# Kernel optimization log

Hardware: AMD Instinct MI355X
Metric: run time of the kernel (lower is better)

The kernel has to match this reference:

```python
import jax, jax.numpy as jnp
import numpy as np

N = 50000   # nodes
E = 800000  # edges
H = 128     # hidden_dim
H2 = H // 2


def setup_inputs() -> dict:
    key = jax.random.key(0)
    ks = jax.random.split(key, 12)
    s = 0.05  # weight scale for numerical sanity
    d = {}
    d['coord_x'] = jax.random.normal(ks[0], (N,), jnp.float32)
    d['coord_y'] = jax.random.normal(ks[1], (N,), jnp.float32)
    d['W1'] = jax.random.normal(ks[2], (3, H), jnp.float32) * s
    d['b1'] = jnp.zeros((H,), jnp.float32)
    d['W2'] = jax.random.normal(ks[3], (H, H), jnp.float32) * s
    d['b2'] = jnp.zeros((H,), jnp.float32)
    d['W3'] = jax.random.normal(ks[4], (H, H), jnp.float32) * s
    d['b3'] = jnp.zeros((H,), jnp.float32)
    d['W4'] = jax.random.normal(ks[5], (H, H), jnp.float32) * s
    d['b4'] = jnp.zeros((H,), jnp.float32)
    d['W5'] = jax.random.normal(ks[6], (H, H), jnp.float32) * s
    d['b5'] = jnp.zeros((H,), jnp.float32)
    d['Wl1'] = jax.random.normal(ks[7], (H, H2), jnp.float32) * s
    d['bl1'] = jnp.zeros((H2,), jnp.float32)
    d['Wl2'] = jax.random.normal(ks[8], (H2, 1), jnp.float32) * s
    d['bl2'] = jnp.zeros((1,), jnp.float32)
    d['src'] = jax.random.randint(ks[9], (E,), 0, N, dtype=jnp.int32)
    d['dst'] = jax.random.randint(ks[10], (E,), 0, N, dtype=jnp.int32)
    return d


def reference(coord_x, coord_y, W1, b1, W2, b2, W3, b3, W4, b4, W5, b5,
              Wl1, bl1, Wl2, bl2, src, dst):
    ones_e = jnp.ones((E,), jnp.float32)
    in_deg = jax.ops.segment_sum(ones_e, dst, num_segments=N)   # [N]
    out_deg = jax.ops.segment_sum(ones_e, src, num_segments=N)  # [N]
    # DGL GraphConv norm='both': D_out^{-1/2} on src side, D_in^{-1/2} on dst side,
    # degrees clamped to min 1.
    norm_s = (jnp.maximum(out_deg, 1.0) ** -0.5)[:, None]  # [N,1]
    norm_d = (jnp.maximum(in_deg, 1.0) ** -0.5)[:, None]   # [N,1]

    def gconv(h, W, b):
        msg = (h * norm_s)[src]                                   # [E,F] gather
        agg = jax.ops.segment_sum(msg, dst, num_segments=N)       # [N,F] scatter-add
        return (agg * norm_d) @ W + b

    # node features: [in_degree, x, y]
    h = jnp.stack([in_deg, coord_x, coord_y], axis=1)  # [N,3]
    for W, b in ((W1, b1), (W2, b2), (W3, b3), (W4, b4), (W5, b5)):
        h = jax.nn.relu(gconv(h, W, b))

    graph_emb = jnp.mean(h, axis=0, keepdims=True)          # [1,H] mean_nodes
    h_emb = jax.nn.relu(graph_emb @ Wl1 + bl1)              # dropout p=0 -> identity
    pred = jax.nn.sigmoid(h_emb @ Wl2 + bl2)                # [1,1]
    return pred, graph_emb, h
```

## Files before the change

kernel.cpp:

```cpp
#include <hip/hip_runtime.h>
#include <hip/hip_bf16.h>
#include <math.h>

#define NN 50000
#define NE 800000
#define HD 128
#define NB 196
#define CAP 5120
#define B1_EPB 1024

typedef __attribute__((ext_vector_type(8))) short bf16x8v;
typedef __attribute__((ext_vector_type(4))) float f32x4v;

static __device__ __forceinline__ unsigned short f2bf(float x) {
    union { float f; unsigned u; } v; v.f = x;
    unsigned r = v.u + 0x7fff + ((v.u >> 16) & 1);
    return (unsigned short)(r >> 16);
}

__global__ __launch_bounds__(256) void bucket_kernel(const int* __restrict__ src,
                                                     const int* __restrict__ dst,
                                                     int* __restrict__ dcur,
                                                     int* __restrict__ scur,
                                                     ushort2* __restrict__ dbucket,
                                                     unsigned short* __restrict__ sbucket) {
    __shared__ int hd[NB], hsb[NB], cd[NB], cs[NB];
    int t = threadIdx.x;
    if (t < NB) { hd[t] = 0; hsb[t] = 0; }
    __syncthreads();
    int d[4], s[4];
    int e0 = blockIdx.x * B1_EPB + t;
    #pragma unroll
    for (int j = 0; j < 4; ++j) {
        int e = e0 + j * 256;
        if (e < NE) {
            d[j] = dst[e]; s[j] = src[e];
            atomicAdd(&hd[d[j] >> 8], 1);
            atomicAdd(&hsb[s[j] >> 8], 1);
        } else d[j] = -1;
    }
    __syncthreads();
    if (t < NB) {
        cd[t] = atomicAdd(&dcur[t], hd[t]);
        cs[t] = atomicAdd(&scur[t], hsb[t]);
    }
    __syncthreads();
    #pragma unroll
    for (int j = 0; j < 4; ++j) {
        if (d[j] >= 0) {
            int b = d[j] >> 8;
            int p = atomicAdd(&cd[b], 1);
            if (p < CAP) dbucket[(long)b * CAP + p] = make_ushort2((unsigned short)d[j],
                                                                   (unsigned short)s[j]);
            int bs = s[j] >> 8;
            int p2 = atomicAdd(&cs[bs], 1);
            if (p2 < CAP) sbucket[(long)bs * CAP + p2] = (unsigned short)s[j];
        }
    }
}

__global__ __launch_bounds__(256) void csr_out_kernel(const ushort2* __restrict__ dbucket,
                                                      const int* __restrict__ dcur,
                                                      const unsigned short* __restrict__ sbucket,
                                                      const int* __restrict__ scur,
                                                      int* __restrict__ row_ptr,
                                                      unsigned short* __restrict__ col,
                                                      int* __restrict__ out_cnt) {
    __shared__ int buf[256];
    __shared__ int hist[256];
    __shared__ int cur[256];
    int k = blockIdx.x, t = threadIdx.x;

    int tot = (t < NB) ? min(dcur[t], CAP) : 0;
    buf[t] = tot;
    __syncthreads();
    for (int o = 1; o < 256; o <<= 1) {
        int a = (t >= o) ? buf[t - o] : 0;
        __syncthreads();
        buf[t] += a;
        __syncthreads();
    }
    int base = (k > 0) ? buf[k - 1] : 0;
    int cnt = min(dcur[k], CAP);

    hist[t] = 0;
    __syncthreads();
    const ushort2* bk = dbucket + (long)k * CAP;
    for (int e = t; e < cnt; e += 256) atomicAdd(&hist[bk[e].x & 255], 1);
    __syncthreads();
    int h = hist[t];

    buf[t] = h;
    __syncthreads();
    for (int o = 1; o < 256; o <<= 1) {
        int a = (t >= o) ? buf[t - o] : 0;
        __syncthreads();
        buf[t] += a;
        __syncthreads();
    }
    int start = base + buf[t] - h;
    int id = (k << 8) + t;
    if (id < NN) row_ptr[id] = start;
    if (k == NB - 1 && t == 0) row_ptr[NN] = base + cnt;
    cur[t] = start;
    __syncthreads();

    for (int e = t; e < cnt; e += 256) {
        ushort2 p = bk[e];
        int pos = atomicAdd(&cur[p.x & 255], 1);
        col[pos] = p.y;
    }

    __syncthreads();
    hist[t] = 0;
    __syncthreads();
    int scnt = min(scur[k], CAP);
    const unsigned short* sk = sbucket + (long)k * CAP;
    for (int e = t; e < scnt; e += 256) atomicAdd(&hist[sk[e] & 255], 1);
    __syncthreads();
    if (id < NN) out_cnt[id] = hist[t];
}

__global__ __launch_bounds__(256) void initw_kernel(const float* __restrict__ cx,
                                                    const float* __restrict__ cy,
                                                    const int* __restrict__ row_ptr,
                                                    const int* __restrict__ out_cnt,
                                                    const float* __restrict__ W2,
                                                    const float* __restrict__ W3,
                                                    const float* __restrict__ W4,
                                                    const float* __restrict__ W5,
                                                    float* __restrict__ norm_s,
                                                    float* __restrict__ norm_d,
                                                    float* __restrict__ h0s,
                                                    unsigned short* __restrict__ Wt,
                                                    float* __restrict__ embsum) {
    int bid = blockIdx.x, t = threadIdx.x;
    if (bid < NB) {
        int i = (bid << 8) + t;
        if (i < NN) {
            float id = (float)(row_ptr[i + 1] - row_ptr[i]);
            float od = (float)out_cnt[i];
            float ns = 1.0f / sqrtf(fmaxf(od, 1.0f));
            norm_s[i] = ns;
            norm_d[i] = 1.0f / sqrtf(fmaxf(id, 1.0f));
            h0s[i * 3 + 0] = id * ns;
            h0s[i * 3 + 1] = cx[i] * ns;
            h0s[i * 3 + 2] = cy[i] * ns;
        }
    } else {
        int gid = ((bid - NB) << 8) + t;
        int l = gid >> 14, idx = gid & 16383;
        int n = idx >> 7, k = idx & 127;
        const float* W = (l == 0) ? W2 : (l == 1) ? W3 : (l == 2) ? W4 : W5;
        Wt[gid] = f2bf(W[k * 128 + n]);
        if (bid == NB && t < 128) embsum[t] = 0.0f;
    }
}

__global__ __launch_bounds__(256) void gather3_kernel(const int* __restrict__ row_ptr,
                                                      const unsigned short* __restrict__ col,
                                                      const float* __restrict__ h0s,
                                                      const float* __restrict__ norm_d,
                                                      float* __restrict__ agg3) {
    int n = blockIdx.x * 256 + threadIdx.x;
    if (n < NN) {
        float a0 = 0.f, a1 = 0.f, a2 = 0.f;
        int end = row_ptr[n + 1];
        for (int e = row_ptr[n]; e < end; ++e) {
            int s = col[e];
            a0 += h0s[s * 3 + 0];
            a1 += h0s[s * 3 + 1];
            a2 += h0s[s * 3 + 2];
        }
        float nd = norm_d[n];
        agg3[n * 3 + 0] = a0 * nd;
        agg3[n * 3 + 1] = a1 * nd;
        agg3[n * 3 + 2] = a2 * nd;
    }
}

__global__ __launch_bounds__(256) void node3_kernel(const float* __restrict__ agg3,
                                                    const float* __restrict__ norm_s,
                                                    const float* __restrict__ W1,
                                                    const float* __restrict__ b1,
                                                    unsigned short* __restrict__ h1s) {
    int gid = blockIdx.x * 256 + threadIdx.x;
    int i = gid >> 7, c = gid & 127;
    if (i < NN) {
        float a0 = agg3[i * 3 + 0];
        float a1 = agg3[i * 3 + 1];
        float a2 = agg3[i * 3 + 2];
        float v = a0 * W1[c] + a1 * W1[128 + c] + a2 * W1[256 + c] + b1[c];
        h1s[i * 128 + c] = f2bf(fmaxf(v, 0.0f) * norm_s[i]);
    }
}

__global__ __launch_bounds__(256) void fused_layer16_kernel(const int* __restrict__ row_ptr,
                                                            const unsigned short* __restrict__ col,
                                                            const unsigned int* __restrict__ hin,
                                                            const float* __restrict__ norm_d,
                                                            const float* __restrict__ norm_s,
                                                            const unsigned short* __restrict__ Wt,
                                                            const float* __restrict__ bias,
                                                            unsigned short* __restrict__ hout) {
    __shared__ unsigned int lA[16][68];
    int t = threadIdx.x;
    int wv = t >> 6, lane = t & 63;
    int m0 = blockIdx.x << 4;

    const unsigned int* hb = hin + lane;
    #pragma unroll
    for (int i = 0; i < 4; ++i) {
        int r = (i << 2) + wv;
        int n = m0 + r;
        int beg = row_ptr[n], end = row_ptr[n + 1];
        float nd = norm_d[n];
        float ax = 0.f, ay = 0.f;
        int e = beg;
        for (; e + 7 < end; e += 8) {
            unsigned u[8];
            #pragma unroll
            for (int j = 0; j < 8; ++j) u[j] = hb[(long)col[e + j] << 6];
            #pragma unroll
            for (int j = 0; j < 8; ++j) {
                ax += __uint_as_float(u[j] << 16);
                ay += __uint_as_float(u[j] & 0xffff0000u);
            }
        }
        for (; e < end; ++e) {
            unsigned u0 = hb[(long)col[e] << 6];
            ax += __uint_as_float(u0 << 16);
            ay += __uint_as_float(u0 & 0xffff0000u);
        }
        lA[r][lane] = (unsigned)f2bf(ax * nd) | ((unsigned)f2bf(ay * nd) << 16);
    }
    __syncthreads();

    int fr = lane & 15, kq = lane >> 4;
    bf16x8v a0 = *(const bf16x8v*)&lA[fr][ 0 + (kq << 2)];
    bf16x8v a1 = *(const bf16x8v*)&lA[fr][16 + (kq << 2)];
    bf16x8v a2 = *(const bf16x8v*)&lA[fr][32 + (kq << 2)];
    bf16x8v a3 = *(const bf16x8v*)&lA[fr][48 + (kq << 2)];

    float4 scv = *(const float4*)(norm_s + m0 + (kq << 2));

    #pragma unroll
    for (int j = 0; j < 2; ++j) {
        int n0 = ((wv << 1) + j) << 4;
        const unsigned short* wb = Wt + ((n0 + fr) << 7) + (kq << 3);
        f32x4v acc = {0.f, 0.f, 0.f, 0.f};
        acc = __builtin_amdgcn_mfma_f32_16x16x32_bf16(a0, *(const bf16x8v*)(wb + 0),  acc, 0, 0, 0);
        acc = __builtin_amdgcn_mfma_f32_16x16x32_bf16(a1, *(const bf16x8v*)(wb + 32), acc, 0, 0, 0);
        acc = __builtin_amdgcn_mfma_f32_16x16x32_bf16(a2, *(const bf16x8v*)(wb + 64), acc, 0, 0, 0);
        acc = __builtin_amdgcn_mfma_f32_16x16x32_bf16(a3, *(const bf16x8v*)(wb + 96), acc, 0, 0, 0);

        int c = n0 + fr;
        float bv = bias[c];
        #pragma unroll
        for (int r = 0; r < 4; ++r) {
            int mr = m0 + (kq << 2) + r;
            float v = fmaxf(acc[r] + bv, 0.f);
            float sc = (r == 0) ? scv.x : (r == 1) ? scv.y : (r == 2) ? scv.z : scv.w;
            hout[((long)mr << 7) + c] = f2bf(v * sc);
        }
    }
}

__global__ __launch_bounds__(256) void gather_bf16_kernel(const int* __restrict__ row_ptr,
                                                          const unsigned short* __restrict__ col,
                                                          const unsigned int* __restrict__ hs2,
                                                          const float* __restrict__ norm_d,
                                                          unsigned int* __restrict__ aggb2) {
    int t = threadIdx.x;
    int wave = t >> 6;
    int lane = t & 63;
    int n = blockIdx.x * 4 + wave;
    if (n >= NN) return;
    int beg = row_ptr[n], end = row_ptr[n + 1];
    float nd = norm_d[n];
    const unsigned int* hb = hs2 + lane;
    float ax = 0.f, ay = 0.f;
    int e = beg;
    for (; e + 7 < end; e += 8) {
        unsigned u[8];
        #pragma unroll
        for (int j = 0; j < 8; ++j) u[j] = hb[(long)col[e + j] << 6];
        #pragma unroll
        for (int j = 0; j < 8; ++j) {
            ax += __uint_as_float(u[j] << 16);
            ay += __uint_as_float(u[j] & 0xffff0000u);
        }
    }
    for (; e < end; ++e) {
        unsigned u0 = hb[(long)col[e] << 6];
        ax += __uint_as_float(u0 << 16);
        ay += __uint_as_float(u0 & 0xffff0000u);
    }
    unsigned po = (unsigned)f2bf(ax * nd) | ((unsigned)f2bf(ay * nd) << 16);
    aggb2[(n << 6) + lane] = po;
}

__global__ __launch_bounds__(256) void gemm_mfma_kernel(const unsigned short* __restrict__ aggb,
                                                        const unsigned short* __restrict__ Wt,
                                                        const float* __restrict__ bias,
                                                        float* __restrict__ out_f32,
                                                        float* __restrict__ embsum) {
    __shared__ unsigned short ldsw[128][136];
    __shared__ float ldscol[4][4][128];

    int t = threadIdx.x;
    int wv = t >> 6, lane = t & 63;
    int fr = lane & 15, kq = lane >> 4;
    int m0 = blockIdx.x * 64 + wv * 16;

    #pragma unroll
    for (int i = 0; i < 8; ++i) {
        int idx = t + 256 * i;
        int r = idx >> 4;
        int c8 = (idx & 15) << 3;
        *(bf16x8v*)(&ldsw[r][c8]) = *(const bf16x8v*)(Wt + (r << 7) + c8);
    }

    int mrow = m0 + fr;
    long abase = (long)((mrow < NN) ? mrow : 0) << 7;
    bf16x8v a0 = *(const bf16x8v*)(aggb + abase + 0  + kq * 8);
    bf16x8v a1 = *(const bf16x8v*)(aggb + abase + 32 + kq * 8);
    bf16x8v a2 = *(const bf16x8v*)(aggb + abase + 64 + kq * 8);
    bf16x8v a3 = *(const bf16x8v*)(aggb + abase + 96 + kq * 8);

    __syncthreads();

    #pragma unroll
    for (int nt = 0; nt < 8; ++nt) {
        int n0 = nt << 4;
        f32x4v acc = {0.f, 0.f, 0.f, 0.f};
        acc = __builtin_amdgcn_mfma_f32_16x16x32_bf16(a0, *(const bf16x8v*)(&ldsw[n0 + fr][0  + kq * 8]), acc, 0, 0, 0);
        acc = __builtin_amdgcn_mfma_f32_16x16x32_bf16(a1, *(const bf16x8v*)(&ldsw[n0 + fr][32 + kq * 8]), acc, 0, 0, 0);
        acc = __builtin_amdgcn_mfma_f32_16x16x32_bf16(a2, *(const bf16x8v*)(&ldsw[n0 + fr][64 + kq * 8]), acc, 0, 0, 0);
        acc = __builtin_amdgcn_mfma_f32_16x16x32_bf16(a3, *(const bf16x8v*)(&ldsw[n0 + fr][96 + kq * 8]), acc, 0, 0, 0);

        int c = n0 + fr;
        float bv = bias[c];
        float cs = 0.f;
        #pragma unroll
        for (int r = 0; r < 4; ++r) {
            int mr = m0 + kq * 4 + r;
            if (mr < NN) {
                float v = fmaxf(acc[r] + bv, 0.f);
                out_f32[((long)mr << 7) + c] = v;
                cs += v;
            }
        }
        ldscol[wv][kq][c] = cs;
    }

    __syncthreads();
    if (t < 128) {
        float s = 0.f;
        #pragma unroll
        for (int w = 0; w < 4; ++w)
            #pragma unroll
            for (int q = 0; q < 4; ++q)
                s += ldscol[w][q][t];
        atomicAdd(&embsum[t], s);
    }
}

__global__ __launch_bounds__(128) void head_kernel(const float* __restrict__ embsum,
                                                   const float* __restrict__ Wl1,
                                                   const float* __restrict__ bl1,
                                                   const float* __restrict__ Wl2,
                                                   const float* __restrict__ bl2,
                                                   float* __restrict__ d_out) {
    __shared__ float emb[128];
    __shared__ float hemb[64];
    int t = threadIdx.x;
    float e = embsum[t] * (1.0f / (float)NN);
    emb[t] = e;
    d_out[1 + t] = e;
    __syncthreads();
    if (t < 64) {
        float acc = bl1[t];
        for (int k = 0; k < 128; ++k)
            acc += emb[k] * Wl1[k * 64 + t];
        hemb[t] = fmaxf(acc, 0.f);
    }
    __syncthreads();
    if (t == 0) {
        float acc = bl2[0];
        for (int j = 0; j < 64; ++j)
            acc += hemb[j] * Wl2[j];
        d_out[0] = 1.0f / (1.0f + expf(-acc));
    }
}

extern "C" void kernel_launch(void* const* d_in, const int* in_sizes, int n_in,
                              void* d_out, int out_size, void* d_ws, size_t ws_size,
                              hipStream_t stream) {
    const float* cx  = (const float*)d_in[0];
    const float* cy  = (const float*)d_in[1];
    const float* W1  = (const float*)d_in[2];
    const float* b1  = (const float*)d_in[3];
    const float* W2  = (const float*)d_in[4];
    const float* b2  = (const float*)d_in[5];
    const float* W3  = (const float*)d_in[6];
    const float* b3  = (const float*)d_in[7];
    const float* W4  = (const float*)d_in[8];
    const float* b4  = (const float*)d_in[9];
    const float* W5  = (const float*)d_in[10];
    const float* b5  = (const float*)d_in[11];
    const float* Wl1 = (const float*)d_in[12];
    const float* bl1 = (const float*)d_in[13];
    const float* Wl2 = (const float*)d_in[14];
    const float* bl2 = (const float*)d_in[15];
    const int*   src = (const int*)d_in[16];
    const int*   dst = (const int*)d_in[17];

    float* out = (float*)d_out;
    float* h_out = out + 129;

    float* ws       = (float*)d_ws;
    float* norm_s   = ws;
    float* norm_d   = ws + NN;
    int*   out_cnt  = (int*)(ws + 2 * NN);
    int*   row_ptr  = (int*)(ws + 3 * NN);
    unsigned short* hsA = (unsigned short*)(ws + 4 * NN + 64);
    unsigned short* hsB = (unsigned short*)(ws + 68 * NN + 64);
    unsigned short* col = (unsigned short*)(ws + 132 * NN + 64);
    float* h0s      = ws + 148 * NN + 64;
    float* agg3     = ws + 151 * NN + 64;
    unsigned short* Wt = (unsigned short*)(ws + 154 * NN + 64);
    float* embsum   = ws + 154 * NN + 64 + 32768;
    int*   dcur     = (int*)(ws + 154 * NN + 33600);
    int*   scur     = dcur + NB;
    ushort2* dbucket = (ushort2*)(ws + 154 * NN + 34048);
    unsigned short* sbucket = (unsigned short*)(ws + 154 * NN + 34048 + NB * CAP);

    hipMemsetAsync(dcur, 0, 2 * NB * sizeof(int), stream);
    bucket_kernel<<<(NE + B1_EPB - 1) / B1_EPB, 256, 0, stream>>>(src, dst, dcur, scur,
                                                                  dbucket, sbucket);
    csr_out_kernel<<<NB, 256, 0, stream>>>(dbucket, dcur, sbucket, scur,
                                           row_ptr, col, out_cnt);

    initw_kernel<<<NB + 256, 256, 0, stream>>>(cx, cy, row_ptr, out_cnt,
                                               W2, W3, W4, W5,
                                               norm_s, norm_d, h0s, Wt, embsum);

    gather3_kernel<<<(NN + 255) / 256, 256, 0, stream>>>(row_ptr, col, h0s, norm_d, agg3);
    node3_kernel<<<(NN * 128) / 256, 256, 0, stream>>>(agg3, norm_s, W1, b1, hsA);

    const float* bs[3] = {b2, b3, b4};
    unsigned short* hcur = hsA;
    unsigned short* hnxt = hsB;
    for (int l = 0; l < 3; ++l) {
        fused_layer16_kernel<<<NN / 16, 256, 0, stream>>>(row_ptr, col,
                                                          (const unsigned int*)hcur,
                                                          norm_d, norm_s,
                                                          Wt + l * 16384, bs[l], hnxt);
        unsigned short* tmp = hcur; hcur = hnxt; hnxt = tmp;
    }

    gather_bf16_kernel<<<(NN + 3) / 4, 256, 0, stream>>>(row_ptr, col,
                                                         (const unsigned int*)hcur,
                                                         norm_d,
                                                         (unsigned int*)hnxt);
    gemm_mfma_kernel<<<(NN + 63) / 64, 256, 0, stream>>>(hnxt, Wt + 3 * 16384, b5,
                                                         h_out, embsum);

    head_kernel<<<1, 128, 0, stream>>>(embsum, Wl1, bl1, Wl2, bl2, out);
}
```

Before: 316.4 us.

## Fuse layer-1 gather with its projection, reuse fused layer kernel for layer 5

```diff
diff --git a/kernel.cpp b/kernel.cpp
--- a/kernel.cpp
+++ b/kernel.cpp
@@ -157,12 +157,24 @@
     }
 }
 
-__global__ __launch_bounds__(256) void gather3_kernel(const int* __restrict__ row_ptr,
-                                                      const unsigned short* __restrict__ col,
-                                                      const float* __restrict__ h0s,
-                                                      const float* __restrict__ norm_d,
-                                                      float* __restrict__ agg3) {
-    int n = blockIdx.x * 256 + threadIdx.x;
+__global__ __launch_bounds__(256) void layer1_kernel(const int* __restrict__ row_ptr,
+                                                     const unsigned short* __restrict__ col,
+                                                     const float* __restrict__ h0s,
+                                                     const float* __restrict__ norm_d,
+                                                     const float* __restrict__ norm_s,
+                                                     const float* __restrict__ W1,
+                                                     const float* __restrict__ b1,
+                                                     unsigned short* __restrict__ h1s) {
+    __shared__ float la3[256][3];
+    __shared__ float lw[3][128];
+    __shared__ float lb[128];
+    int t = threadIdx.x;
+    int n0 = blockIdx.x << 8;
+    if (t < 128) {
+        lw[0][t] = W1[t]; lw[1][t] = W1[128 + t]; lw[2][t] = W1[256 + t];
+        lb[t] = b1[t];
+    }
+    int n = n0 + t;
     if (n < NN) {
         float a0 = 0.f, a1 = 0.f, a2 = 0.f;
         int end = row_ptr[n + 1];
@@ -173,25 +185,19 @@
             a2 += h0s[s * 3 + 2];
         }
         float nd = norm_d[n];
-        agg3[n * 3 + 0] = a0 * nd;
-        agg3[n * 3 + 1] = a1 * nd;
-        agg3[n * 3 + 2] = a2 * nd;
-    }
-}
-
-__global__ __launch_bounds__(256) void node3_kernel(const float* __restrict__ agg3,
-                                                    const float* __restrict__ norm_s,
-                                                    const float* __restrict__ W1,
-                                                    const float* __restrict__ b1,
-                                                    unsigned short* __restrict__ h1s) {
-    int gid = blockIdx.x * 256 + threadIdx.x;
-    int i = gid >> 7, c = gid & 127;
-    if (i < NN) {
-        float a0 = agg3[i * 3 + 0];
-        float a1 = agg3[i * 3 + 1];
-        float a2 = agg3[i * 3 + 2];
-        float v = a0 * W1[c] + a1 * W1[128 + c] + a2 * W1[256 + c] + b1[c];
-        h1s[i * 128 + c] = f2bf(fmaxf(v, 0.0f) * norm_s[i]);
+        la3[t][0] = a0 * nd; la3[t][1] = a1 * nd; la3[t][2] = a2 * nd;
+    }
+    __syncthreads();
+    #pragma unroll 4
+    for (int i = 0; i < 128; ++i) {
+        int idx = (i << 8) + t;
+        int r = idx >> 7, c = idx & 127;
+        int nn = n0 + r;
+        if (nn < NN) {
+            float v = la3[r][0] * lw[0][c] + la3[r][1] * lw[1][c]
+                    + la3[r][2] * lw[2][c] + lb[c];
+            h1s[((long)nn << 7) + c] = f2bf(fmaxf(v, 0.f) * norm_s[nn]);
+        }
     }
 }
 
@@ -202,21 +208,40 @@
                                                             const float* __restrict__ norm_s,
                                                             const unsigned short* __restrict__ Wt,
                                                             const float* __restrict__ bias,
-                                                            unsigned short* __restrict__ hout) {
+                                                            unsigned short* __restrict__ hout,
+                                                            float* __restrict__ out_f32,
+                                                            float* __restrict__ embsum) {
     __shared__ unsigned int lA[16][68];
+    __shared__ float ldscol[4][128];
+    __shared__ int cursor;
     int t = threadIdx.x;
     int wv = t >> 6, lane = t & 63;
     int m0 = blockIdx.x << 4;
 
+    if (t == 0) cursor = 0;
+    __syncthreads();
+
     const unsigned int* hb = hin + lane;
-    #pragma unroll
-    for (int i = 0; i < 4; ++i) {
-        int r = (i << 2) + wv;
+    for (;;) {
+        int r0 = 0;
+        if (lane == 0) r0 = atomicAdd(&cursor, 1);
+        int r = __shfl(r0, 0);
+        if (r >= 16) break;
         int n = m0 + r;
         int beg = row_ptr[n], end = row_ptr[n + 1];
         float nd = norm_d[n];
         float ax = 0.f, ay = 0.f;
         int e = beg;
+        for (; e + 15 < end; e += 16) {
+            unsigned u[16];
+            #pragma unroll
+            for (int j = 0; j < 16; ++j) u[j] = hb[(long)col[e + j] << 6];
+            #pragma unroll
+            for (int j = 0; j < 16; ++j) {
+                ax += __uint_as_float(u[j] << 16);
+                ay += __uint_as_float(u[j] & 0xffff0000u);
+            }
+        }
         for (; e + 7 < end; e += 8) {
             unsigned u[8];
             #pragma unroll
@@ -242,7 +267,8 @@
     bf16x8v a2 = *(const bf16x8v*)&lA[fr][32 + (kq << 2)];
     bf16x8v a3 = *(const bf16x8v*)&lA[fr][48 + (kq << 2)];
 
-    float4 scv = *(const float4*)(norm_s + m0 + (kq << 2));
+    float4 scv = make_float4(1.f, 1.f, 1.f, 1.f);
+    if (!out_f32) scv = *(const float4*)(norm_s + m0 + (kq << 2));
 
     #pragma unroll
     for (int j = 0; j < 2; ++j) {
@@ -256,113 +282,33 @@
 
         int c = n0 + fr;
         float bv = bias[c];
-        #pragma unroll
-        for (int r = 0; r < 4; ++r) {
-            int mr = m0 + (kq << 2) + r;
-            float v = fmaxf(acc[r] + bv, 0.f);
-            float sc = (r == 0) ? scv.x : (r == 1) ? scv.y : (r == 2) ? scv.z : scv.w;
-            hout[((long)mr << 7) + c] = f2bf(v * sc);
-        }
-    }
-}
-
-__global__ __launch_bounds__(256) void gather_bf16_kernel(const int* __restrict__ row_ptr,
-                                                          const unsigned short* __restrict__ col,
-                                                          const unsigned int* __restrict__ hs2,
-                                                          const float* __restrict__ norm_d,
-                                                          unsigned int* __restrict__ aggb2) {
-    int t = threadIdx.x;
-    int wave = t >> 6;
-    int lane = t & 63;
-    int n = blockIdx.x * 4 + wave;
-    if (n >= NN) return;
-    int beg = row_ptr[n], end = row_ptr[n + 1];
-    float nd = norm_d[n];
-    const unsigned int* hb = hs2 + lane;
-    float ax = 0.f, ay = 0.f;
-    int e = beg;
-    for (; e + 7 < end; e += 8) {
-        unsigned u[8];
-        #pragma unroll
-        for (int j = 0; j < 8; ++j) u[j] = hb[(long)col[e + j] << 6];
-        #pragma unroll
-        for (int j = 0; j < 8; ++j) {
-            ax += __uint_as_float(u[j] << 16);
-            ay += __uint_as_float(u[j] & 0xffff0000u);
-        }
-    }
-    for (; e < end; ++e) {
-        unsigned u0 = hb[(long)col[e] << 6];
-        ax += __uint_as_float(u0 << 16);
-        ay += __uint_as_float(u0 & 0xffff0000u);
-    }
-    unsigned po = (unsigned)f2bf(ax * nd) | ((unsigned)f2bf(ay * nd) << 16);
-    aggb2[(n << 6) + lane] = po;
-}
-
-__global__ __launch_bounds__(256) void gemm_mfma_kernel(const unsigned short* __restrict__ aggb,
-                                                        const unsigned short* __restrict__ Wt,
-                                                        const float* __restrict__ bias,
-                                                        float* __restrict__ out_f32,
-                                                        float* __restrict__ embsum) {
-    __shared__ unsigned short ldsw[128][136];
-    __shared__ float ldscol[4][4][128];
-
-    int t = threadIdx.x;
-    int wv = t >> 6, lane = t & 63;
-    int fr = lane & 15, kq = lane >> 4;
-    int m0 = blockIdx.x * 64 + wv * 16;
-
-    #pragma unroll
-    for (int i = 0; i < 8; ++i) {
-        int idx = t + 256 * i;
-        int r = idx >> 4;
-        int c8 = (idx & 15) << 3;
-        *(bf16x8v*)(&ldsw[r][c8]) = *(const bf16x8v*)(Wt + (r << 7) + c8);
-    }
-
-    int mrow = m0 + fr;
-    long abase = (long)((mrow < NN) ? mrow : 0) << 7;
-    bf16x8v a0 = *(const bf16x8v*)(aggb + abase + 0  + kq * 8);
-    bf16x8v a1 = *(const bf16x8v*)(aggb + abase + 32 + kq * 8);
-    bf16x8v a2 = *(const bf16x8v*)(aggb + abase + 64 + kq * 8);
-    bf16x8v a3 = *(const bf16x8v*)(aggb + abase + 96 + kq * 8);
-
-    __syncthreads();
-
-    #pragma unroll
-    for (int nt = 0; nt < 8; ++nt) {
-        int n0 = nt << 4;
-        f32x4v acc = {0.f, 0.f, 0.f, 0.f};
-        acc = __builtin_amdgcn_mfma_f32_16x16x32_bf16(a0, *(const bf16x8v*)(&ldsw[n0 + fr][0  + kq * 8]), acc, 0, 0, 0);
-        acc = __builtin_amdgcn_mfma_f32_16x16x32_bf16(a1, *(const bf16x8v*)(&ldsw[n0 + fr][32 + kq * 8]), acc, 0, 0, 0);
-        acc = __builtin_amdgcn_mfma_f32_16x16x32_bf16(a2, *(const bf16x8v*)(&ldsw[n0 + fr][64 + kq * 8]), acc, 0, 0, 0);
-        acc = __builtin_amdgcn_mfma_f32_16x16x32_bf16(a3, *(const bf16x8v*)(&ldsw[n0 + fr][96 + kq * 8]), acc, 0, 0, 0);
-
-        int c = n0 + fr;
-        float bv = bias[c];
-        float cs = 0.f;
-        #pragma unroll
-        for (int r = 0; r < 4; ++r) {
-            int mr = m0 + kq * 4 + r;
-            if (mr < NN) {
+        if (out_f32) {
+            float cs = 0.f;
+            #pragma unroll
+            for (int r = 0; r < 4; ++r) {
+                int mr = m0 + (kq << 2) + r;
                 float v = fmaxf(acc[r] + bv, 0.f);
                 out_f32[((long)mr << 7) + c] = v;
                 cs += v;
             }
-        }
-        ldscol[wv][kq][c] = cs;
-    }
-
-    __syncthreads();
-    if (t < 128) {
-        float s = 0.f;
-        #pragma unroll
-        for (int w = 0; w < 4; ++w)
-            #pragma unroll
-            for (int q = 0; q < 4; ++q)
-                s += ldscol[w][q][t];
-        atomicAdd(&embsum[t], s);
+            ldscol[kq][c] = cs;
+        } else {
+            #pragma unroll
+            for (int r = 0; r < 4; ++r) {
+                int mr = m0 + (kq << 2) + r;
+                float v = fmaxf(acc[r] + bv, 0.f);
+                float sc = (r == 0) ? scv.x : (r == 1) ? scv.y : (r == 2) ? scv.z : scv.w;
+                hout[((long)mr << 7) + c] = f2bf(v * sc);
+            }
+        }
+    }
+
+    if (out_f32) {
+        __syncthreads();
+        if (t < 128) {
+            float s = ldscol[0][t] + ldscol[1][t] + ldscol[2][t] + ldscol[3][t];
+            atomicAdd(&embsum[t], s);
+        }
     }
 }
 
@@ -428,7 +374,6 @@
     unsigned short* hsB = (unsigned short*)(ws + 68 * NN + 64);
     unsigned short* col = (unsigned short*)(ws + 132 * NN + 64);
     float* h0s      = ws + 148 * NN + 64;
-    float* agg3     = ws + 151 * NN + 64;
     unsigned short* Wt = (unsigned short*)(ws + 154 * NN + 64);
     float* embsum   = ws + 154 * NN + 64 + 32768;
     int*   dcur     = (int*)(ws + 154 * NN + 33600);
@@ -446,26 +391,22 @@
                                                W2, W3, W4, W5,
                                                norm_s, norm_d, h0s, Wt, embsum);
 
-    gather3_kernel<<<(NN + 255) / 256, 256, 0, stream>>>(row_ptr, col, h0s, norm_d, agg3);
-    node3_kernel<<<(NN * 128) / 256, 256, 0, stream>>>(agg3, norm_s, W1, b1, hsA);
-
-    const float* bs[3] = {b2, b3, b4};
+    layer1_kernel<<<(NN + 255) / 256, 256, 0, stream>>>(row_ptr, col, h0s,
+                                                        norm_d, norm_s, W1, b1, hsA);
+
+    const float* bs[4] = {b2, b3, b4, b5};
     unsigned short* hcur = hsA;
     unsigned short* hnxt = hsB;
-    for (int l = 0; l < 3; ++l) {
-        fused_layer16_kernel<<<NN / 16, 256, 0, stream>>>(row_ptr, col,
-                                                          (const unsigned int*)hcur,
-                                                          norm_d, norm_s,
-                                                          Wt + l * 16384, bs[l], hnxt);
+    for (int l = 0; l < 4; ++l) {
+        bool last = (l == 3);
+        fused_layer16_kernel<<<NN / 16, 256, 0, stream>>>(
+            row_ptr, col, (const unsigned int*)hcur, norm_d, norm_s,
+            Wt + l * 16384, bs[l],
+            last ? nullptr : hnxt,
+            last ? h_out : nullptr,
+            last ? embsum : nullptr);
         unsigned short* tmp = hcur; hcur = hnxt; hnxt = tmp;
     }
 
-    gather_bf16_kernel<<<(NN + 3) / 4, 256, 0, stream>>>(row_ptr, col,
-                                                         (const unsigned int*)hcur,
-                                                         norm_d,
-                                                         (unsigned int*)hnxt);
-    gemm_mfma_kernel<<<(NN + 63) / 64, 256, 0, stream>>>(hnxt, Wt + 3 * 16384, b5,
-                                                         h_out, embsum);
-
     head_kernel<<<1, 128, 0, stream>>>(embsum, Wl1, bl1, Wl2, bl2, out);
 }
```

New measurement: 344.7 us. 1.09x slower.
